# Kernel optimization log

Measured on AMD Instinct MI355X. Metric: run time of the kernel, lower is better.

The kernel has to match this reference:

```python
import jax, jax.numpy as jnp
import numpy as np

EPS = 1e-5

def _ln(x, g, b):
    m = x.mean(-1, keepdims=True)
    v = x.var(-1, keepdims=True)
    return (x - m) / jnp.sqrt(v + EPS) * g + b

def _ln_na(x):
    m = x.mean(-1, keepdims=True)
    v = x.var(-1, keepdims=True)
    return (x - m) / jnp.sqrt(v + EPS)

def setup_inputs() -> dict:
    key = jax.random.key(0)
    ks = jax.random.split(key, 12)
    B, J, D, H, E, Z = 128, 4096, 64, 128, 256, 32
    s = 0.05
    return {
        "x": jax.random.normal(ks[0], (B, J), jnp.float32),
        "mask": jax.random.randint(ks[1], (B, J), 0, 2, jnp.int32),
        "feature_embedding": jax.random.normal(ks[2], (J, D), jnp.float32),
        "hW1": jax.random.normal(ks[3], (1 + D, H), jnp.float32) * s,
        "hb1": jnp.zeros((H,), jnp.float32),
        "hg1": jnp.ones((H,), jnp.float32),
        "hbt1": jnp.zeros((H,), jnp.float32),
        "hW2": jax.random.normal(ks[4], (H, D), jnp.float32) * s,
        "hb2": jnp.zeros((D,), jnp.float32),
        "hg2": jnp.ones((D,), jnp.float32),
        "hbt2": jnp.zeros((D,), jnp.float32),
        "eW1": jax.random.normal(ks[5], (D, E), jnp.float32) * s,
        "eb1": jnp.zeros((E,), jnp.float32),
        "eW2": jax.random.normal(ks[6], (E, 2 * Z), jnp.float32) * s,
        "eb2": jnp.zeros((2 * Z,), jnp.float32),
    }

def reference(x, mask, feature_embedding, hW1, hb1, hg1, hbt1, hW2, hb2, hg2, hbt2, eW1, eb1, eW2, eb2):
    B, J = x.shape
    D = feature_embedding.shape[1]
    m = (mask > 0).astype(x.dtype)  # (B, J)
    # per-(b,j) MLP on [x_bj, F_j]; masked entries are zeroed before pooling,
    # which equals the original gather-then-MLP-then-sum over observed entries.
    F = jnp.broadcast_to(feature_embedding[None], (B, J, D))
    h_in = jnp.concatenate([x[..., None], F], axis=-1)        # (B, J, 1+D)
    h = jax.nn.relu(_ln(h_in @ hW1 + hb1, hg1, hbt1))          # (B, J, H)
    h = jax.nn.relu(_ln(h @ hW2 + hb2, hg2, hbt2))             # (B, J, D)
    pooled = jnp.einsum('bjd,bj->bd', h, m)                    # sum over observed
    cnt = jnp.maximum(m.sum(-1, keepdims=True), 1.0)
    c = pooled / cnt                                           # mean pool; zeros if no obs
    # FCLayers (2 layers, LayerNorm w/o affine, ReLU each layer)
    e = jax.nn.relu(_ln_na(c @ eW1 + eb1))                     # (B, E)
    out = jax.nn.relu(_ln_na(e @ eW2 + eb2))                   # (B, 2Z)
    mu, logvar = jnp.split(out, 2, axis=-1)
    return (mu, logvar)
```

## Files before the change

### kernel.cpp

```cpp
#include <hip/hip_runtime.h>
#include <hip/hip_bf16.h>

#define B_  128
#define J_  4096
#define D_  64
#define H_  128
#define E_  256
#define Z_  32

typedef __attribute__((ext_vector_type(8))) short short8;
typedef __attribute__((ext_vector_type(4))) float floatx4;

#define OFF_G      0u
#define OFF_GSTATS 2097152u
#define OFF_SCAL   2162688u
#define OFF_W0C    2162944u
#define OFF_C3     2163456u
#define OFF_W2F    2163968u
#define OFF_POOL   2180352u

static __device__ __forceinline__ unsigned pk2(float a, float b) {
    __hip_bfloat162 t = __float22bfloat162_rn(make_float2(a, b));
    union { __hip_bfloat162 h; unsigned u; } c; c.h = t; return c.u;
}

__global__ __launch_bounds__(128) void g_kernel(
    const float* __restrict__ F, const float* __restrict__ hW1,
    const float* __restrict__ hb1, const float* __restrict__ hg1,
    float* __restrict__ Gp, float4* __restrict__ Gstats)
{
    const int j = blockIdx.x;
    const int h = threadIdx.x;
    const float* frow = F + (size_t)j * D_;
    float a0 = hb1[h], a1 = 0.f, a2 = 0.f, a3 = 0.f;
#pragma unroll
    for (int d = 0; d < D_; d += 4) {
        a0 = fmaf(frow[d + 0], hW1[(d + 1) * H_ + h], a0);
        a1 = fmaf(frow[d + 1], hW1[(d + 2) * H_ + h], a1);
        a2 = fmaf(frow[d + 2], hW1[(d + 3) * H_ + h], a2);
        a3 = fmaf(frow[d + 3], hW1[(d + 4) * H_ + h], a3);
    }
    const float acc = (a0 + a1) + (a2 + a3);

    const float w0h = hW1[h];
    float s1 = acc, s2 = w0h * acc, s3 = acc * acc;
#pragma unroll
    for (int off = 32; off; off >>= 1) {
        s1 += __shfl_xor(s1, off);
        s2 += __shfl_xor(s2, off);
        s3 += __shfl_xor(s3, off);
    }
    __shared__ float red[6];
    if ((h & 63) == 0) {
        int w = h >> 6;
        red[w*3+0] = s1; red[w*3+1] = s2; red[w*3+2] = s3;
    }
    __syncthreads();
    const float inv = 1.f / (float)H_;
    const float mG = (red[0] + red[3]) * inv;
    if (h == 0)
        Gstats[j] = make_float4(mG, (red[1]+red[4])*inv, (red[2]+red[5])*inv, 0.f);
    Gp[j * H_ + h] = (acc - mG) * hg1[h];
}

__global__ __launch_bounds__(256) void prep_kernel(
    const float* __restrict__ hW1, const float* __restrict__ hg1,
    const float* __restrict__ hbt1, const float* __restrict__ hW2,
    float* __restrict__ scal, float* __restrict__ w0c, float* __restrict__ c3,
    uint4* __restrict__ w2f, float4* __restrict__ pooled4)
{
    const int t = threadIdx.x;
    if (blockIdx.x > 0) {
        pooled4[(blockIdx.x - 1) * 256 + t] = make_float4(0.f, 0.f, 0.f, 0.f);
        return;
    }

    __shared__ float sred[4];
    if (t < H_) {
        const float w0h = hW1[t];
        float s = w0h, q = w0h * w0h;
#pragma unroll
        for (int off = 32; off; off >>= 1) {
            s += __shfl_xor(s, off);
            q += __shfl_xor(q, off);
        }
        if ((t & 63) == 0) { sred[(t >> 6) * 2] = s; sred[(t >> 6) * 2 + 1] = q; }
    }
    __syncthreads();
    const float mw0  = (sred[0] + sred[2]) * (1.f / (float)H_);
    const float ew02 = (sred[1] + sred[3]) * (1.f / (float)H_);
    if (t == 0) { scal[0] = mw0; scal[1] = ew02; }
    if (t < H_) {
        w0c[t] = (hW1[t] - mw0) * hg1[t];
        c3[t]  = hbt1[t];
    }

    const int lane = t & 63, wq = t >> 6;
    const int quad = lane >> 4, col = lane & 15;
    for (int f = wq; f < 16; f += 4) {
        const int kstep = f >> 2, nt = f & 3;
        const int kbase = kstep * 32 + quad * 8;
        const int n = nt * 16 + col;
        unsigned r[4];
#pragma unroll
        for (int p = 0; p < 4; p++)
            r[p] = pk2(hW2[(kbase + 2*p) * D_ + n], hW2[(kbase + 2*p + 1) * D_ + n]);
        w2f[f * 64 + lane] = make_uint4(r[0], r[1], r[2], r[3]);
    }
}

#define TPW 2
#define BB  4

__global__ __launch_bounds__(256, 2) void main_kernel(
    const float* __restrict__ x, const int* __restrict__ mask,
    const float* __restrict__ Gp, const float4* __restrict__ Gstats,
    const float* __restrict__ scal,
    const float* __restrict__ w0c, const float* __restrict__ c3,
    const uint4* __restrict__ w2f,
    const float* __restrict__ hb2, const float* __restrict__ hg2,
    const float* __restrict__ hbt2,
    float* __restrict__ pooled)
{
    const int tid  = threadIdx.x;
    const int lane = tid & 63;
    const int wv   = tid >> 6;
    const int quad = lane >> 4;
    const int col  = lane & 15;
    const int b0   = blockIdx.y * BB;

    short8 w2r[16];
#pragma unroll
    for (int f = 0; f < 16; f++) {
        union { uint4 v; short8 s; } c; c.v = w2f[f * 64 + lane];
        w2r[f] = c.s;
    }
    float4 wc[4][2], cc[4][2];
#pragma unroll
    for (int k = 0; k < 4; k++) {
        wc[k][0] = ((const float4*)(w0c + k*32 + quad*8))[0];
        wc[k][1] = ((const float4*)(w0c + k*32 + quad*8))[1];
        cc[k][0] = ((const float4*)(c3  + k*32 + quad*8))[0];
        cc[k][1] = ((const float4*)(c3  + k*32 + quad*8))[1];
    }
    float hb2v[4], g2v[4], bt2v[4];
#pragma unroll
    for (int nt = 0; nt < 4; nt++) {
        hb2v[nt] = hb2[nt*16 + col];
        g2v[nt]  = hg2[nt*16 + col];
        bt2v[nt] = hbt2[nt*16 + col];
    }
    const float mw0s  = scal[0];
    const float ew02s = scal[1];

    float pool[BB][4];
#pragma unroll
    for (int bb = 0; bb < BB; bb++)
#pragma unroll
        for (int nt = 0; nt < 4; nt++) pool[bb][nt] = 0.f;

    for (int t = 0; t < TPW; t++) {
        const int tIdx = (blockIdx.x * 4 + wv) * TPW + t;
        const int j0   = tIdx * 16;
        const int rowA = j0 + col;

        const float4 gs = Gstats[rowA];
        float xv[BB]; int4 mk[BB];
#pragma unroll
        for (int bb = 0; bb < BB; bb++) {
            xv[bb] = x[(size_t)(b0 + bb) * J_ + rowA];
            mk[bb] = *(const int4*)(mask + (size_t)(b0 + bb) * J_ + j0 + quad * 4);
        }
        const float* gpr = Gp + rowA * H_ + quad * 8;
        float4 ga[4][2];
#pragma unroll
        for (int k = 0; k < 4; k++) {
            ga[k][0] = ((const float4*)(gpr + k*32))[0];
            ga[k][1] = ((const float4*)(gpr + k*32))[1];
        }

#pragma unroll
        for (int bb = 0; bb < BB; bb++) {
            const float xA = xv[bb];
            const float mean = fmaf(xA, mw0s, gs.x);
            const float eh2  = fmaf(xA, fmaf(xA, ew02s, 2.f * gs.y), gs.z);
            const float r1   = rsqrtf(fmaf(-mean, mean, eh2) + 1e-5f);

            floatx4 acc[4];
#pragma unroll
            for (int nt = 0; nt < 4; nt++) acc[nt] = (floatx4){0.f, 0.f, 0.f, 0.f};

#pragma unroll
            for (int k = 0; k < 4; k++) {
                const float h0 = fmaxf(0.f, fmaf(fmaf(xA, wc[k][0].x, ga[k][0].x), r1, cc[k][0].x));
                const float h1 = fmaxf(0.f, fmaf(fmaf(xA, wc[k][0].y, ga[k][0].y), r1, cc[k][0].y));
                const float h2 = fmaxf(0.f, fmaf(fmaf(xA, wc[k][0].z, ga[k][0].z), r1, cc[k][0].z));
                const float h3 = fmaxf(0.f, fmaf(fmaf(xA, wc[k][0].w, ga[k][0].w), r1, cc[k][0].w));
                const float h4 = fmaxf(0.f, fmaf(fmaf(xA, wc[k][1].x, ga[k][1].x), r1, cc[k][1].x));
                const float h5 = fmaxf(0.f, fmaf(fmaf(xA, wc[k][1].y, ga[k][1].y), r1, cc[k][1].y));
                const float h6 = fmaxf(0.f, fmaf(fmaf(xA, wc[k][1].z, ga[k][1].z), r1, cc[k][1].z));
                const float h7 = fmaxf(0.f, fmaf(fmaf(xA, wc[k][1].w, ga[k][1].w), r1, cc[k][1].w));
                union { unsigned u[4]; short8 s; } af;
                af.u[0] = pk2(h0, h1);
                af.u[1] = pk2(h2, h3);
                af.u[2] = pk2(h4, h5);
                af.u[3] = pk2(h6, h7);
                acc[0] = __builtin_amdgcn_mfma_f32_16x16x32_bf16(af.s, w2r[k*4+0], acc[0], 0, 0, 0);
                acc[1] = __builtin_amdgcn_mfma_f32_16x16x32_bf16(af.s, w2r[k*4+1], acc[1], 0, 0, 0);
                acc[2] = __builtin_amdgcn_mfma_f32_16x16x32_bf16(af.s, w2r[k*4+2], acc[2], 0, 0, 0);
                acc[3] = __builtin_amdgcn_mfma_f32_16x16x32_bf16(af.s, w2r[k*4+3], acc[3], 0, 0, 0);
            }

            float sa[4], qa[4];
#pragma unroll
            for (int r = 0; r < 4; r++) {
                const float v0 = acc[0][r] + hb2v[0];
                const float v1 = acc[1][r] + hb2v[1];
                const float v2 = acc[2][r] + hb2v[2];
                const float v3 = acc[3][r] + hb2v[3];
                acc[0][r] = v0; acc[1][r] = v1; acc[2][r] = v2; acc[3][r] = v3;
                sa[r] = (v0 + v1) + (v2 + v3);
                qa[r] = fmaf(v0, v0, fmaf(v1, v1, fmaf(v2, v2, v3 * v3)));
            }
#pragma unroll
            for (int m = 1; m < 16; m <<= 1) {
#pragma unroll
                for (int r = 0; r < 4; r++) {
                    sa[r] += __shfl_xor(sa[r], m);
                    qa[r] += __shfl_xor(qa[r], m);
                }
            }
            float mrr[4];
            mrr[0] = (mk[bb].x > 0) ? 1.f : 0.f;
            mrr[1] = (mk[bb].y > 0) ? 1.f : 0.f;
            mrr[2] = (mk[bb].z > 0) ? 1.f : 0.f;
            mrr[3] = (mk[bb].w > 0) ? 1.f : 0.f;
#pragma unroll
            for (int r = 0; r < 4; r++) {
                const float m2 = sa[r] * (1.f / 64.f);
                const float v2 = fmaf(-m2, m2, qa[r] * (1.f / 64.f));
                const float r2 = rsqrtf(v2 + 1e-5f);
#pragma unroll
                for (int nt = 0; nt < 4; nt++) {
                    const float rg  = r2 * g2v[nt];
                    const float off = fmaf(-m2, rg, bt2v[nt]);
                    const float o   = fmaxf(0.f, fmaf(acc[nt][r], rg, off));
                    pool[bb][nt] = fmaf(mrr[r], o, pool[bb][nt]);
                }
            }
        }
    }

#pragma unroll
    for (int m = 16; m < 64; m <<= 1)
#pragma unroll
        for (int bb = 0; bb < BB; bb++)
#pragma unroll
            for (int nt = 0; nt < 4; nt++)
                pool[bb][nt] += __shfl_xor(pool[bb][nt], m);

    if (lane < 16) {
#pragma unroll
        for (int bb = 0; bb < BB; bb++)
#pragma unroll
            for (int nt = 0; nt < 4; nt++)
                atomicAdd(&pooled[(size_t)(b0 + bb) * D_ + nt * 16 + lane], pool[bb][nt]);
    }
}

__global__ __launch_bounds__(256) void final_kernel(
    const float* __restrict__ pooled, const int* __restrict__ mask,
    const float* __restrict__ eW1, const float* __restrict__ eb1,
    const float* __restrict__ eW2, const float* __restrict__ eb2,
    float* __restrict__ out)
{
    __shared__ float c_lds[D_];
    __shared__ float e_lds[E_];
    __shared__ float red[8];
    __shared__ float redc[4];
    const int b = blockIdx.x;
    const int t = threadIdx.x;
    const int lane = t & 63, wid = t >> 6;

    {
        const int4* mrow = (const int4*)(mask + (size_t)b * J_);
        int s = 0;
#pragma unroll
        for (int i = 0; i < 4; i++) {
            const int4 v = mrow[t * 4 + i];
            s += (v.x > 0) + (v.y > 0) + (v.z > 0) + (v.w > 0);
        }
        float fs = (float)s;
#pragma unroll
        for (int off = 32; off; off >>= 1) fs += __shfl_xor(fs, off);
        if (lane == 0) redc[wid] = fs;
    }
    __syncthreads();
    const float cn = fmaxf((redc[0] + redc[1]) + (redc[2] + redc[3]), 1.f);
    if (t < D_) c_lds[t] = pooled[(size_t)b * D_ + t] / cn;
    __syncthreads();

    float acc = eb1[t];
#pragma unroll
    for (int d = 0; d < D_; d++)
        acc = fmaf(c_lds[d], eW1[(size_t)d * E_ + t], acc);

    float s = acc, s2 = acc * acc;
#pragma unroll
    for (int off = 32; off; off >>= 1) {
        s  += __shfl_xor(s, off);
        s2 += __shfl_xor(s2, off);
    }
    if ((t & 63) == 0) { red[wid * 2] = s; red[wid * 2 + 1] = s2; }
    __syncthreads();
    s  = red[0] + red[2] + red[4] + red[6];
    s2 = red[1] + red[3] + red[5] + red[7];
    const float m = s * (1.f / (float)E_);
    const float v = fmaf(-m, m, s2 * (1.f / (float)E_));
    const float r = rsqrtf(v + 1e-5f);
    e_lds[t] = fmaxf(0.f, (acc - m) * r);
    __syncthreads();

    if (t < 64) {
        float a2 = eb2[t];
#pragma unroll 8
        for (int k = 0; k < E_; k++)
            a2 = fmaf(e_lds[k], eW2[(size_t)k * 64 + t], a2);

        float u = a2, u2 = a2 * a2;
#pragma unroll
        for (int off = 32; off; off >>= 1) {
            u  += __shfl_xor(u, off);
            u2 += __shfl_xor(u2, off);
        }
        const float m2 = u * (1.f / 64.f);
        const float v2 = fmaf(-m2, m2, u2 * (1.f / 64.f));
        const float r2 = rsqrtf(v2 + 1e-5f);
        const float o  = fmaxf(0.f, (a2 - m2) * r2);
        if (t < Z_) out[(size_t)b * Z_ + t] = o;
        else        out[(size_t)B_ * Z_ + (size_t)b * Z_ + (t - Z_)] = o;
    }
}

extern "C" void kernel_launch(void* const* d_in, const int* in_sizes, int n_in,
                              void* d_out, int out_size, void* d_ws, size_t ws_size,
                              hipStream_t stream) {
    const float* x    = (const float*)d_in[0];
    const int*   mask = (const int*)d_in[1];
    const float* F    = (const float*)d_in[2];
    const float* hW1  = (const float*)d_in[3];
    const float* hb1  = (const float*)d_in[4];
    const float* hg1  = (const float*)d_in[5];
    const float* hbt1 = (const float*)d_in[6];
    const float* hW2  = (const float*)d_in[7];
    const float* hb2  = (const float*)d_in[8];
    const float* hg2  = (const float*)d_in[9];
    const float* hbt2 = (const float*)d_in[10];
    const float* eW1  = (const float*)d_in[11];
    const float* eb1  = (const float*)d_in[12];
    const float* eW2  = (const float*)d_in[13];
    const float* eb2  = (const float*)d_in[14];
    float* out = (float*)d_out;

    char* ws = (char*)d_ws;
    float*  Gp     = (float*)(ws + OFF_G);
    float4* Gstats = (float4*)(ws + OFF_GSTATS);
    float*  scal   = (float*)(ws + OFF_SCAL);
    float*  w0c    = (float*)(ws + OFF_W0C);
    float*  c3     = (float*)(ws + OFF_C3);
    uint4*  w2f    = (uint4*)(ws + OFF_W2F);
    float*  pooled = (float*)(ws + OFF_POOL);

    g_kernel<<<J_, 128, 0, stream>>>(F, hW1, hb1, hg1, Gp, Gstats);
    prep_kernel<<<9, 256, 0, stream>>>(hW1, hg1, hbt1, hW2, scal, w0c, c3, w2f,
                                       (float4*)pooled);
    main_kernel<<<dim3(J_ / (16 * 4 * TPW), B_ / BB), 256, 0, stream>>>(
        x, mask, Gp, Gstats, scal, w0c, c3, w2f, hb2, hg2, hbt2, pooled);
    final_kernel<<<B_, E_, 0, stream>>>(pooled, mask, eW1, eb1, eW2, eb2, out);
}
```

Measured before the change: 142.0 us.

## Fuse prep kernels and fold final MLP into main kernel via last-block ticket

```diff
diff --git a/kernel.cpp b/kernel.cpp
--- a/kernel.cpp
+++ b/kernel.cpp
@@ -18,19 +18,79 @@
 #define OFF_C3     2163456u
 #define OFF_W2F    2163968u
 #define OFF_POOL   2180352u
-
+#define OFF_CNT    2213120u
+#define OFF_TICK   2213632u
+
+#if defined(__has_builtin)
+#if __has_builtin(__builtin_amdgcn_cvt_pk_bf16_f32)
+#define HAVE_CVT_PK_BF16 1
+#endif
+#endif
+
+#ifdef HAVE_CVT_PK_BF16
+typedef __attribute__((ext_vector_type(2))) __bf16 bf16x2;
+static __device__ __forceinline__ unsigned pk2(float a, float b) {
+    return __builtin_bit_cast(unsigned, __builtin_amdgcn_cvt_pk_bf16_f32(a, b));
+}
+#else
 static __device__ __forceinline__ unsigned pk2(float a, float b) {
     __hip_bfloat162 t = __float22bfloat162_rn(make_float2(a, b));
     union { __hip_bfloat162 h; unsigned u; } c; c.h = t; return c.u;
 }
-
-__global__ __launch_bounds__(128) void g_kernel(
+#endif
+
+__global__ __launch_bounds__(128) void pre_kernel(
     const float* __restrict__ F, const float* __restrict__ hW1,
     const float* __restrict__ hb1, const float* __restrict__ hg1,
-    float* __restrict__ Gp, float4* __restrict__ Gstats)
+    const float* __restrict__ hbt1, const float* __restrict__ hW2,
+    float* __restrict__ Gp, float4* __restrict__ Gstats,
+    float* __restrict__ scal, float* __restrict__ w0c, float* __restrict__ c3,
+    uint4* __restrict__ w2f, float4* __restrict__ zero4)
 {
-    const int j = blockIdx.x;
-    const int h = threadIdx.x;
+    __shared__ float red[6];
+    const int bid = blockIdx.x;
+    const int t = threadIdx.x;
+
+    if (bid >= 4097) {
+        const int base = (bid - 4097) * 256;
+        zero4[base + t]       = make_float4(0.f, 0.f, 0.f, 0.f);
+        zero4[base + 128 + t] = make_float4(0.f, 0.f, 0.f, 0.f);
+        return;
+    }
+
+    if (bid == 4096) {
+        const float w0h = hW1[t];
+        float s = w0h, q = w0h * w0h;
+#pragma unroll
+        for (int off = 32; off; off >>= 1) {
+            s += __shfl_xor(s, off);
+            q += __shfl_xor(q, off);
+        }
+        if ((t & 63) == 0) { red[(t >> 6) * 2] = s; red[(t >> 6) * 2 + 1] = q; }
+        __syncthreads();
+        const float mw0  = (red[0] + red[2]) * (1.f / (float)H_);
+        const float ew02 = (red[1] + red[3]) * (1.f / (float)H_);
+        if (t == 0) { scal[0] = mw0; scal[1] = ew02; }
+        w0c[t] = (hW1[t] - mw0) * hg1[t];
+        c3[t]  = hbt1[t];
+
+        const int lane = t & 63, half = t >> 6;
+        const int quad = lane >> 4, col = lane & 15;
+        for (int f = half; f < 16; f += 2) {
+            const int kstep = f >> 2, nt = f & 3;
+            const int kbase = kstep * 32 + quad * 8;
+            const int n = nt * 16 + col;
+            unsigned r[4];
+#pragma unroll
+            for (int p = 0; p < 4; p++)
+                r[p] = pk2(hW2[(kbase + 2*p) * D_ + n], hW2[(kbase + 2*p + 1) * D_ + n]);
+            w2f[f * 64 + lane] = make_uint4(r[0], r[1], r[2], r[3]);
+        }
+        return;
+    }
+
+    const int j = bid;
+    const int h = t;
     const float* frow = F + (size_t)j * D_;
     float a0 = hb1[h], a1 = 0.f, a2 = 0.f, a3 = 0.f;
 #pragma unroll
@@ -50,7 +110,6 @@
         s2 += __shfl_xor(s2, off);
         s3 += __shfl_xor(s3, off);
     }
-    __shared__ float red[6];
     if ((h & 63) == 0) {
         int w = h >> 6;
         red[w*3+0] = s1; red[w*3+1] = s2; red[w*3+2] = s3;
@@ -63,56 +122,10 @@
     Gp[j * H_ + h] = (acc - mG) * hg1[h];
 }
 
-__global__ __launch_bounds__(256) void prep_kernel(
-    const float* __restrict__ hW1, const float* __restrict__ hg1,
-    const float* __restrict__ hbt1, const float* __restrict__ hW2,
-    float* __restrict__ scal, float* __restrict__ w0c, float* __restrict__ c3,
-    uint4* __restrict__ w2f, float4* __restrict__ pooled4)
-{
-    const int t = threadIdx.x;
-    if (blockIdx.x > 0) {
-        pooled4[(blockIdx.x - 1) * 256 + t] = make_float4(0.f, 0.f, 0.f, 0.f);
-        return;
-    }
-
-    __shared__ float sred[4];
-    if (t < H_) {
-        const float w0h = hW1[t];
-        float s = w0h, q = w0h * w0h;
-#pragma unroll
-        for (int off = 32; off; off >>= 1) {
-            s += __shfl_xor(s, off);
-            q += __shfl_xor(q, off);
-        }
-        if ((t & 63) == 0) { sred[(t >> 6) * 2] = s; sred[(t >> 6) * 2 + 1] = q; }
-    }
-    __syncthreads();
-    const float mw0  = (sred[0] + sred[2]) * (1.f / (float)H_);
-    const float ew02 = (sred[1] + sred[3]) * (1.f / (float)H_);
-    if (t == 0) { scal[0] = mw0; scal[1] = ew02; }
-    if (t < H_) {
-        w0c[t] = (hW1[t] - mw0) * hg1[t];
-        c3[t]  = hbt1[t];
-    }
-
-    const int lane = t & 63, wq = t >> 6;
-    const int quad = lane >> 4, col = lane & 15;
-    for (int f = wq; f < 16; f += 4) {
-        const int kstep = f >> 2, nt = f & 3;
-        const int kbase = kstep * 32 + quad * 8;
-        const int n = nt * 16 + col;
-        unsigned r[4];
-#pragma unroll
-        for (int p = 0; p < 4; p++)
-            r[p] = pk2(hW2[(kbase + 2*p) * D_ + n], hW2[(kbase + 2*p + 1) * D_ + n]);
-        w2f[f * 64 + lane] = make_uint4(r[0], r[1], r[2], r[3]);
-    }
-}
-
 #define TPW 2
 #define BB  4
 
-__global__ __launch_bounds__(256, 2) void main_kernel(
+__global__ __launch_bounds__(256, 4) void main_kernel(
     const float* __restrict__ x, const int* __restrict__ mask,
     const float* __restrict__ Gp, const float4* __restrict__ Gstats,
     const float* __restrict__ scal,
@@ -120,8 +133,16 @@
     const uint4* __restrict__ w2f,
     const float* __restrict__ hb2, const float* __restrict__ hg2,
     const float* __restrict__ hbt2,
-    float* __restrict__ pooled)
+    const float* __restrict__ eW1, const float* __restrict__ eb1,
+    const float* __restrict__ eW2, const float* __restrict__ eb2,
+    float* __restrict__ pooled, float* __restrict__ cnt,
+    int* __restrict__ tickets, float* __restrict__ out)
 {
+    __shared__ float c_lds[D_];
+    __shared__ float e_lds[E_];
+    __shared__ float hred[8];
+    __shared__ int   tick_s;
+
     const int tid  = threadIdx.x;
     const int lane = tid & 63;
     const int wv   = tid >> 6;
@@ -153,11 +174,13 @@
     const float mw0s  = scal[0];
     const float ew02s = scal[1];
 
-    float pool[BB][4];
-#pragma unroll
-    for (int bb = 0; bb < BB; bb++)
+    float pool[BB][4], cna[BB];
+#pragma unroll
+    for (int bb = 0; bb < BB; bb++) {
+        cna[bb] = 0.f;
 #pragma unroll
         for (int nt = 0; nt < 4; nt++) pool[bb][nt] = 0.f;
+    }
 
     for (int t = 0; t < TPW; t++) {
         const int tIdx = (blockIdx.x * 4 + wv) * TPW + t;
@@ -248,97 +271,89 @@
                     pool[bb][nt] = fmaf(mrr[r], o, pool[bb][nt]);
                 }
             }
-        }
-    }
-
-#pragma unroll
-    for (int m = 16; m < 64; m <<= 1)
-#pragma unroll
-        for (int bb = 0; bb < BB; bb++)
+            cna[bb] += (mrr[0] + mrr[1]) + (mrr[2] + mrr[3]);
+        }
+    }
+
+#pragma unroll
+    for (int m = 16; m < 64; m <<= 1) {
+#pragma unroll
+        for (int bb = 0; bb < BB; bb++) {
 #pragma unroll
             for (int nt = 0; nt < 4; nt++)
                 pool[bb][nt] += __shfl_xor(pool[bb][nt], m);
-
+            cna[bb] += __shfl_xor(cna[bb], m);
+        }
+    }
     if (lane < 16) {
 #pragma unroll
-        for (int bb = 0; bb < BB; bb++)
+        for (int bb = 0; bb < BB; bb++) {
 #pragma unroll
             for (int nt = 0; nt < 4; nt++)
                 atomicAdd(&pooled[(size_t)(b0 + bb) * D_ + nt * 16 + lane], pool[bb][nt]);
-    }
-}
-
-__global__ __launch_bounds__(256) void final_kernel(
-    const float* __restrict__ pooled, const int* __restrict__ mask,
-    const float* __restrict__ eW1, const float* __restrict__ eb1,
-    const float* __restrict__ eW2, const float* __restrict__ eb2,
-    float* __restrict__ out)
-{
-    __shared__ float c_lds[D_];
-    __shared__ float e_lds[E_];
-    __shared__ float red[8];
-    __shared__ float redc[4];
-    const int b = blockIdx.x;
-    const int t = threadIdx.x;
-    const int lane = t & 63, wid = t >> 6;
-
-    {
-        const int4* mrow = (const int4*)(mask + (size_t)b * J_);
-        int s = 0;
-#pragma unroll
-        for (int i = 0; i < 4; i++) {
-            const int4 v = mrow[t * 4 + i];
-            s += (v.x > 0) + (v.y > 0) + (v.z > 0) + (v.w > 0);
-        }
-        float fs = (float)s;
-#pragma unroll
-        for (int off = 32; off; off >>= 1) fs += __shfl_xor(fs, off);
-        if (lane == 0) redc[wid] = fs;
-    }
+            if (lane == 0) atomicAdd(&cnt[b0 + bb], cna[bb]);
+        }
+    }
+
+    __threadfence();
     __syncthreads();
-    const float cn = fmaxf((redc[0] + redc[1]) + (redc[2] + redc[3]), 1.f);
-    if (t < D_) c_lds[t] = pooled[(size_t)b * D_ + t] / cn;
+    if (tid == 0) tick_s = atomicAdd(&tickets[blockIdx.y], 1);
     __syncthreads();
-
-    float acc = eb1[t];
-#pragma unroll
-    for (int d = 0; d < D_; d++)
-        acc = fmaf(c_lds[d], eW1[(size_t)d * E_ + t], acc);
-
-    float s = acc, s2 = acc * acc;
-#pragma unroll
-    for (int off = 32; off; off >>= 1) {
-        s  += __shfl_xor(s, off);
-        s2 += __shfl_xor(s2, off);
-    }
-    if ((t & 63) == 0) { red[wid * 2] = s; red[wid * 2 + 1] = s2; }
-    __syncthreads();
-    s  = red[0] + red[2] + red[4] + red[6];
-    s2 = red[1] + red[3] + red[5] + red[7];
-    const float m = s * (1.f / (float)E_);
-    const float v = fmaf(-m, m, s2 * (1.f / (float)E_));
-    const float r = rsqrtf(v + 1e-5f);
-    e_lds[t] = fmaxf(0.f, (acc - m) * r);
-    __syncthreads();
-
-    if (t < 64) {
-        float a2 = eb2[t];
+    if (tick_s != 31) return;
+    __threadfence();
+
+    const int t256 = tid;
+    const int wid = tid >> 6;
+    for (int bb = 0; bb < BB; bb++) {
+        const int b = b0 + bb;
+        if (t256 == 0) c_lds[0] = fmaxf(atomicAdd(&cnt[b], 0.f), 1.f);
+        __syncthreads();
+        const float cn = c_lds[0];
+        __syncthreads();
+        if (t256 < D_) c_lds[t256] = atomicAdd(&pooled[(size_t)b * D_ + t256], 0.f) / cn;
+        __syncthreads();
+
+        float acc = eb1[t256];
+#pragma unroll
+        for (int d = 0; d < D_; d++)
+            acc = fmaf(c_lds[d], eW1[(size_t)d * E_ + t256], acc);
+
+        float s = acc, s2 = acc * acc;
+#pragma unroll
+        for (int off = 32; off; off >>= 1) {
+            s  += __shfl_xor(s, off);
+            s2 += __shfl_xor(s2, off);
+        }
+        if ((t256 & 63) == 0) { hred[wid * 2] = s; hred[wid * 2 + 1] = s2; }
+        __syncthreads();
+        s  = hred[0] + hred[2] + hred[4] + hred[6];
+        s2 = hred[1] + hred[3] + hred[5] + hred[7];
+        const float m = s * (1.f / (float)E_);
+        const float v = fmaf(-m, m, s2 * (1.f / (float)E_));
+        const float r = rsqrtf(v + 1e-5f);
+        e_lds[t256] = fmaxf(0.f, (acc - m) * r);
+        __syncthreads();
+
+        if (t256 < 64) {
+            float a2 = eb2[t256];
 #pragma unroll 8
-        for (int k = 0; k < E_; k++)
-            a2 = fmaf(e_lds[k], eW2[(size_t)k * 64 + t], a2);
-
-        float u = a2, u2 = a2 * a2;
-#pragma unroll
-        for (int off = 32; off; off >>= 1) {
-            u  += __shfl_xor(u, off);
-            u2 += __shfl_xor(u2, off);
-        }
-        const float m2 = u * (1.f / 64.f);
-        const float v2 = fmaf(-m2, m2, u2 * (1.f / 64.f));
-        const float r2 = rsqrtf(v2 + 1e-5f);
-        const float o  = fmaxf(0.f, (a2 - m2) * r2);
-        if (t < Z_) out[(size_t)b * Z_ + t] = o;
-        else        out[(size_t)B_ * Z_ + (size_t)b * Z_ + (t - Z_)] = o;
+            for (int k = 0; k < E_; k++)
+                a2 = fmaf(e_lds[k], eW2[(size_t)k * 64 + t256], a2);
+
+            float u = a2, u2 = a2 * a2;
+#pragma unroll
+            for (int off = 32; off; off >>= 1) {
+                u  += __shfl_xor(u, off);
+                u2 += __shfl_xor(u2, off);
+            }
+            const float m2 = u * (1.f / 64.f);
+            const float v2 = fmaf(-m2, m2, u2 * (1.f / 64.f));
+            const float r2 = rsqrtf(v2 + 1e-5f);
+            const float o  = fmaxf(0.f, (a2 - m2) * r2);
+            if (t256 < Z_) out[(size_t)b * Z_ + t256] = o;
+            else           out[(size_t)B_ * Z_ + (size_t)b * Z_ + (t256 - Z_)] = o;
+        }
+        __syncthreads();
     }
 }
 
@@ -370,11 +385,13 @@
     float*  c3     = (float*)(ws + OFF_C3);
     uint4*  w2f    = (uint4*)(ws + OFF_W2F);
     float*  pooled = (float*)(ws + OFF_POOL);
-
-    g_kernel<<<J_, 128, 0, stream>>>(F, hW1, hb1, hg1, Gp, Gstats);
-    prep_kernel<<<9, 256, 0, stream>>>(hW1, hg1, hbt1, hW2, scal, w0c, c3, w2f,
-                                       (float4*)pooled);
+    float*  cnt    = (float*)(ws + OFF_CNT);
+    int*    tick   = (int*)(ws + OFF_TICK);
+
+    pre_kernel<<<J_ + 10, 128, 0, stream>>>(F, hW1, hb1, hg1, hbt1, hW2,
+                                            Gp, Gstats, scal, w0c, c3, w2f,
+                                            (float4*)pooled);
     main_kernel<<<dim3(J_ / (16 * 4 * TPW), B_ / BB), 256, 0, stream>>>(
-        x, mask, Gp, Gstats, scal, w0c, c3, w2f, hb2, hg2, hbt2, pooled);
-    final_kernel<<<B_, E_, 0, stream>>>(pooled, mask, eW1, eb1, eW2, eb2, out);
-}
+        x, mask, Gp, Gstats, scal, w0c, c3, w2f, hb2, hg2, hbt2,
+        eW1, eb1, eW2, eb2, pooled, cnt, tick, out);
+}
```

After: 436.3 us. 3.07x slower.

## Merge G and prep kernels, process four features per block

Applied to the files above, without the earlier changes.

```diff
diff --git a/kernel.cpp b/kernel.cpp
--- a/kernel.cpp
+++ b/kernel.cpp
@@ -19,64 +19,43 @@
 #define OFF_W2F    2163968u
 #define OFF_POOL   2180352u
 
+#if defined(__has_builtin)
+#if __has_builtin(__builtin_amdgcn_cvt_pk_bf16_f32)
+#define HAVE_CVT_PK_BF16 1
+#endif
+#endif
+
+#ifdef HAVE_CVT_PK_BF16
+static __device__ __forceinline__ unsigned pk2(float a, float b) {
+    return __builtin_bit_cast(unsigned, __builtin_amdgcn_cvt_pk_bf16_f32(a, b));
+}
+#else
 static __device__ __forceinline__ unsigned pk2(float a, float b) {
     __hip_bfloat162 t = __float22bfloat162_rn(make_float2(a, b));
     union { __hip_bfloat162 h; unsigned u; } c; c.h = t; return c.u;
 }
-
-__global__ __launch_bounds__(128) void g_kernel(
+#endif
+
+__global__ __launch_bounds__(128) void pre_kernel(
     const float* __restrict__ F, const float* __restrict__ hW1,
     const float* __restrict__ hb1, const float* __restrict__ hg1,
-    float* __restrict__ Gp, float4* __restrict__ Gstats)
+    const float* __restrict__ hbt1, const float* __restrict__ hW2,
+    float* __restrict__ Gp, float4* __restrict__ Gstats,
+    float* __restrict__ scal, float* __restrict__ w0c, float* __restrict__ c3,
+    uint4* __restrict__ w2f, float4* __restrict__ zero4)
 {
-    const int j = blockIdx.x;
-    const int h = threadIdx.x;
-    const float* frow = F + (size_t)j * D_;
-    float a0 = hb1[h], a1 = 0.f, a2 = 0.f, a3 = 0.f;
-#pragma unroll
-    for (int d = 0; d < D_; d += 4) {
-        a0 = fmaf(frow[d + 0], hW1[(d + 1) * H_ + h], a0);
-        a1 = fmaf(frow[d + 1], hW1[(d + 2) * H_ + h], a1);
-        a2 = fmaf(frow[d + 2], hW1[(d + 3) * H_ + h], a2);
-        a3 = fmaf(frow[d + 3], hW1[(d + 4) * H_ + h], a3);
-    }
-    const float acc = (a0 + a1) + (a2 + a3);
-
-    const float w0h = hW1[h];
-    float s1 = acc, s2 = w0h * acc, s3 = acc * acc;
-#pragma unroll
-    for (int off = 32; off; off >>= 1) {
-        s1 += __shfl_xor(s1, off);
-        s2 += __shfl_xor(s2, off);
-        s3 += __shfl_xor(s3, off);
-    }
-    __shared__ float red[6];
-    if ((h & 63) == 0) {
-        int w = h >> 6;
-        red[w*3+0] = s1; red[w*3+1] = s2; red[w*3+2] = s3;
-    }
-    __syncthreads();
-    const float inv = 1.f / (float)H_;
-    const float mG = (red[0] + red[3]) * inv;
-    if (h == 0)
-        Gstats[j] = make_float4(mG, (red[1]+red[4])*inv, (red[2]+red[5])*inv, 0.f);
-    Gp[j * H_ + h] = (acc - mG) * hg1[h];
-}
-
-__global__ __launch_bounds__(256) void prep_kernel(
-    const float* __restrict__ hW1, const float* __restrict__ hg1,
-    const float* __restrict__ hbt1, const float* __restrict__ hW2,
-    float* __restrict__ scal, float* __restrict__ w0c, float* __restrict__ c3,
-    uint4* __restrict__ w2f, float4* __restrict__ pooled4)
-{
+    __shared__ float red[24];
+    const int bid = blockIdx.x;
     const int t = threadIdx.x;
-    if (blockIdx.x > 0) {
-        pooled4[(blockIdx.x - 1) * 256 + t] = make_float4(0.f, 0.f, 0.f, 0.f);
+
+    if (bid > 1024) {
+        const int base = (bid - 1025) * 256;
+        zero4[base + t]       = make_float4(0.f, 0.f, 0.f, 0.f);
+        zero4[base + 128 + t] = make_float4(0.f, 0.f, 0.f, 0.f);
         return;
     }
 
-    __shared__ float sred[4];
-    if (t < H_) {
+    if (bid == 1024) {
         const float w0h = hW1[t];
         float s = w0h, q = w0h * w0h;
 #pragma unroll
@@ -84,28 +63,72 @@
             s += __shfl_xor(s, off);
             q += __shfl_xor(q, off);
         }
-        if ((t & 63) == 0) { sred[(t >> 6) * 2] = s; sred[(t >> 6) * 2 + 1] = q; }
-    }
-    __syncthreads();
-    const float mw0  = (sred[0] + sred[2]) * (1.f / (float)H_);
-    const float ew02 = (sred[1] + sred[3]) * (1.f / (float)H_);
-    if (t == 0) { scal[0] = mw0; scal[1] = ew02; }
-    if (t < H_) {
+        if ((t & 63) == 0) { red[(t >> 6) * 2] = s; red[(t >> 6) * 2 + 1] = q; }
+        __syncthreads();
+        const float mw0  = (red[0] + red[2]) * (1.f / (float)H_);
+        const float ew02 = (red[1] + red[3]) * (1.f / (float)H_);
+        if (t == 0) { scal[0] = mw0; scal[1] = ew02; }
         w0c[t] = (hW1[t] - mw0) * hg1[t];
         c3[t]  = hbt1[t];
-    }
-
-    const int lane = t & 63, wq = t >> 6;
-    const int quad = lane >> 4, col = lane & 15;
-    for (int f = wq; f < 16; f += 4) {
-        const int kstep = f >> 2, nt = f & 3;
-        const int kbase = kstep * 32 + quad * 8;
-        const int n = nt * 16 + col;
-        unsigned r[4];
-#pragma unroll
-        for (int p = 0; p < 4; p++)
-            r[p] = pk2(hW2[(kbase + 2*p) * D_ + n], hW2[(kbase + 2*p + 1) * D_ + n]);
-        w2f[f * 64 + lane] = make_uint4(r[0], r[1], r[2], r[3]);
+
+        const int lane = t & 63, half = t >> 6;
+        const int quad = lane >> 4, col = lane & 15;
+        for (int f = half; f < 16; f += 2) {
+            const int kstep = f >> 2, nt = f & 3;
+            const int kbase = kstep * 32 + quad * 8;
+            const int n = nt * 16 + col;
+            unsigned r[4];
+#pragma unroll
+            for (int p = 0; p < 4; p++)
+                r[p] = pk2(hW2[(kbase + 2*p) * D_ + n], hW2[(kbase + 2*p + 1) * D_ + n]);
+            w2f[f * 64 + lane] = make_uint4(r[0], r[1], r[2], r[3]);
+        }
+        return;
+    }
+
+    const int j0 = bid * 4;
+    const int h  = t;
+    const float* f0 = F + (size_t)(j0 + 0) * D_;
+    const float* f1 = F + (size_t)(j0 + 1) * D_;
+    const float* f2p = F + (size_t)(j0 + 2) * D_;
+    const float* f3 = F + (size_t)(j0 + 3) * D_;
+    const float bias = hb1[h];
+    float a0 = bias, a1 = bias, a2 = bias, a3 = bias;
+#pragma unroll
+    for (int d = 0; d < D_; d++) {
+        const float w = hW1[(d + 1) * H_ + h];
+        a0 = fmaf(f0[d], w, a0);
+        a1 = fmaf(f1[d], w, a1);
+        a2 = fmaf(f2p[d], w, a2);
+        a3 = fmaf(f3[d], w, a3);
+    }
+
+    const float w0h = hW1[h];
+    const float g1h = hg1[h];
+    float accs[4] = {a0, a1, a2, a3};
+#pragma unroll
+    for (int q = 0; q < 4; q++) {
+        float s1 = accs[q], s2 = w0h * accs[q], s3 = accs[q] * accs[q];
+#pragma unroll
+        for (int off = 32; off; off >>= 1) {
+            s1 += __shfl_xor(s1, off);
+            s2 += __shfl_xor(s2, off);
+            s3 += __shfl_xor(s3, off);
+        }
+        if ((h & 63) == 0) {
+            int w = h >> 6;
+            red[q*6 + w*3 + 0] = s1; red[q*6 + w*3 + 1] = s2; red[q*6 + w*3 + 2] = s3;
+        }
+    }
+    __syncthreads();
+    const float inv = 1.f / (float)H_;
+#pragma unroll
+    for (int q = 0; q < 4; q++) {
+        const float mG = (red[q*6 + 0] + red[q*6 + 3]) * inv;
+        if (h == 0)
+            Gstats[j0 + q] = make_float4(mG, (red[q*6+1] + red[q*6+4]) * inv,
+                                             (red[q*6+2] + red[q*6+5]) * inv, 0.f);
+        Gp[(j0 + q) * H_ + h] = (accs[q] - mG) * g1h;
     }
 }
 
@@ -287,7 +310,7 @@
         int s = 0;
 #pragma unroll
         for (int i = 0; i < 4; i++) {
-            const int4 v = mrow[t * 4 + i];
+            const int4 v = mrow[i * 256 + t];
             s += (v.x > 0) + (v.y > 0) + (v.z > 0) + (v.w > 0);
         }
         float fs = (float)s;
@@ -371,9 +394,9 @@
     uint4*  w2f    = (uint4*)(ws + OFF_W2F);
     float*  pooled = (float*)(ws + OFF_POOL);
 
-    g_kernel<<<J_, 128, 0, stream>>>(F, hW1, hb1, hg1, Gp, Gstats);
-    prep_kernel<<<9, 256, 0, stream>>>(hW1, hg1, hbt1, hW2, scal, w0c, c3, w2f,
-                                       (float4*)pooled);
+    pre_kernel<<<1033, 128, 0, stream>>>(F, hW1, hb1, hg1, hbt1, hW2,
+                                         Gp, Gstats, scal, w0c, c3, w2f,
+                                         (float4*)pooled);
     main_kernel<<<dim3(J_ / (16 * 4 * TPW), B_ / BB), 256, 0, stream>>>(
         x, mask, Gp, Gstats, scal, w0c, c3, w2f, hb2, hg2, hbt2, pooled);
     final_kernel<<<B_, E_, 0, stream>>>(pooled, mask, eW1, eb1, eW2, eb2, out);
```

Result: faster. 138.0 us (-2.8%).
